# Kernel tuning notes

Measured on AMD Instinct MI355X. Metric: run time of the kernel, lower is better.

## Reference

```python
import jax, jax.numpy as jnp
import numpy as np

N_NODES = 20000
N_EDGES = 640000
IN_F = 128
CL1_F = 128
CL2_F = 128
OUT_F = 2


def setup_inputs() -> dict:
    key = jax.random.key(0)
    ks = jax.random.split(key, 8)
    x = jax.random.normal(ks[0], (N_NODES, IN_F), dtype=jnp.float32)
    edge_index = jax.random.randint(ks[1], (2, N_EDGES), 0, N_NODES, dtype=jnp.int64)
    s1 = 1.0 / np.sqrt(IN_F)
    s2 = 1.0 / np.sqrt(CL1_F)
    s3 = 1.0 / np.sqrt(CL2_F)
    W1 = jax.random.uniform(ks[2], (IN_F, CL1_F), jnp.float32, -s1, s1)
    b1 = jax.random.uniform(ks[3], (CL1_F,), jnp.float32, -s1, s1)
    W2 = jax.random.uniform(ks[4], (CL1_F, CL2_F), jnp.float32, -s2, s2)
    b2 = jax.random.uniform(ks[5], (CL2_F,), jnp.float32, -s2, s2)
    W3 = jax.random.uniform(ks[6], (CL2_F, OUT_F), jnp.float32, -s3, s3)
    b3 = jax.random.uniform(ks[7], (OUT_F,), jnp.float32, -s3, s3)
    return {"x": x, "edge_index": edge_index, "W1": W1, "b1": b1,
            "W2": W2, "b2": b2, "W3": W3, "b3": b3}


def _scatter_mean(feat_src, src, dst, n_nodes):
    # out[i] = mean over edges e with dst[e]==i of feat_src gathered at src[e]
    msg = feat_src[src]                                   # [E, F] gather
    summed = jax.ops.segment_sum(msg, dst, num_segments=n_nodes)  # [N, F]
    ones = jnp.ones((src.shape[0],), dtype=feat_src.dtype)
    cnt = jax.ops.segment_sum(ones, dst, num_segments=n_nodes)    # [N]
    return summed / jnp.maximum(cnt, 1.0)[:, None]


def _mpnn_layer(x, src, dst, W, b, n_nodes):
    aggr = _scatter_mean(x, src, dst, n_nodes)
    return jax.nn.relu(aggr @ W + b)


def reference(x, edge_index, W1, b1, W2, b2, W3, b3):
    src, dst = edge_index[0], edge_index[1]
    n = x.shape[0]
    h = _mpnn_layer(x, src, dst, W1, b1, n)   # conv1 (update relu); extra relu is no-op
    h = _mpnn_layer(h, src, dst, W2, b2, n)   # conv2
    # dropout in eval mode is identity
    return h @ W3 + b3
```

## Files before the change

kernel.cpp:

```cpp
#include <hip/hip_runtime.h>

#define N_NODES 20000
#define N_EDGES 640000
#define F 128
#define CAP 128
#define GEMM_BLOCKS (N_NODES / 32)
#define SCAT_BLOCKS 2560
#define SCAT_STRIDE (SCAT_BLOCKS / 8 * 256)
#define NODES_PER_XCD (N_NODES / 8)


__global__ __launch_bounds__(256)
void gemm_bucket_kernel(const float* __restrict__ A, const float* __restrict__ W,
                        float* __restrict__ C,
                        const int* __restrict__ src, const int* __restrict__ dst,
                        int* __restrict__ cnt, unsigned short* __restrict__ bucket) {
    __shared__ float As[32][F + 4];
    int tid = threadIdx.x;
    int bid = blockIdx.x;

    if (bid >= GEMM_BLOCKS) {
        int s   = bid - GEMM_BLOCKS;
        int g   = bid & 7;
        int idx = s >> 3;
        int lo  = g * NODES_PER_XCD;
        int hi  = lo + NODES_PER_XCD;
        for (int e = idx * 256 + tid; e < N_EDGES; e += SCAT_STRIDE) {
            int d  = dst[e];
            int sv = src[e];
            if (d >= lo && d < hi) {
                int pos = atomicAdd(&cnt[d], 1);
                if (pos < CAP) bucket[(size_t)d * CAP + pos] = (unsigned short)sv;
            }
        }
        return;
    }

    int row0 = bid * 32;
    const float4* A4 = (const float4*)(A + (size_t)row0 * F);
    for (int i = tid; i < 32 * 32; i += 256) {
        float4 v = A4[i];
        int r = i >> 5, c4 = (i & 31) * 4;
        *(float4*)&As[r][c4] = v;
    }
    __syncthreads();

    int tx = tid & 31, ty = tid >> 5;
    int c0 = tx * 4, r0 = ty * 4;
    float acc[4][4] = {};

    for (int k = 0; k < F; k += 4) {
        float4 a4[4];
#pragma unroll
        for (int i = 0; i < 4; ++i) a4[i] = *(const float4*)&As[r0 + i][k];
#pragma unroll
        for (int u = 0; u < 4; ++u) {
            float4 w = *(const float4*)(W + (size_t)(k + u) * F + c0);
#pragma unroll
            for (int i = 0; i < 4; ++i) {
                float a = (u == 0) ? a4[i].x : (u == 1) ? a4[i].y : (u == 2) ? a4[i].z : a4[i].w;
                acc[i][0] += a * w.x;
                acc[i][1] += a * w.y;
                acc[i][2] += a * w.z;
                acc[i][3] += a * w.w;
            }
        }
    }

#pragma unroll
    for (int i = 0; i < 4; ++i) {
        float4 o;
        o.x = acc[i][0]; o.y = acc[i][1]; o.z = acc[i][2]; o.w = acc[i][3];
        *(float4*)(C + (size_t)(row0 + r0 + i) * F + c0) = o;
    }
}

__global__ __launch_bounds__(256)
void gemm_kernel(const float* __restrict__ A, const float* __restrict__ W,
                 float* __restrict__ C) {
    __shared__ float As[32][F + 4];
    int tid  = threadIdx.x;
    int row0 = blockIdx.x * 32;

    const float4* A4 = (const float4*)(A + (size_t)row0 * F);
    for (int i = tid; i < 32 * 32; i += 256) {
        float4 v = A4[i];
        int r = i >> 5, c4 = (i & 31) * 4;
        *(float4*)&As[r][c4] = v;
    }
    __syncthreads();

    int tx = tid & 31, ty = tid >> 5;
    int c0 = tx * 4, r0 = ty * 4;
    float acc[4][4] = {};

    for (int k = 0; k < F; k += 4) {
        float4 a4[4];
#pragma unroll
        for (int i = 0; i < 4; ++i) a4[i] = *(const float4*)&As[r0 + i][k];
#pragma unroll
        for (int u = 0; u < 4; ++u) {
            float4 w = *(const float4*)(W + (size_t)(k + u) * F + c0);
#pragma unroll
            for (int i = 0; i < 4; ++i) {
                float a = (u == 0) ? a4[i].x : (u == 1) ? a4[i].y : (u == 2) ? a4[i].z : a4[i].w;
                acc[i][0] += a * w.x;
                acc[i][1] += a * w.y;
                acc[i][2] += a * w.z;
                acc[i][3] += a * w.w;
            }
        }
    }

#pragma unroll
    for (int i = 0; i < 4; ++i) {
        float4 o;
        o.x = acc[i][0]; o.y = acc[i][1]; o.z = acc[i][2]; o.w = acc[i][3];
        *(float4*)(C + (size_t)(row0 + r0 + i) * F + c0) = o;
    }
}

__device__ __forceinline__ float4 slice_gather(const float4* __restrict__ fb,
                                               int packed, int deg, int r) {
    float4 acc; acc.x = acc.y = acc.z = acc.w = 0.f;
    int nchunks = deg >> 3;
    int sh  = r >> 1;
    int sel = r & 1;
    int c = 0;
    for (; c + 4 <= nchunks; c += 4) {
        int w0 = __shfl(packed, (c << 2) + sh);
        int w1 = __shfl(packed, ((c + 1) << 2) + sh);
        int w2 = __shfl(packed, ((c + 2) << 2) + sh);
        int w3 = __shfl(packed, ((c + 3) << 2) + sh);
        int i0 = sel ? ((w0 >> 16) & 0xffff) : (w0 & 0xffff);
        int i1 = sel ? ((w1 >> 16) & 0xffff) : (w1 & 0xffff);
        int i2 = sel ? ((w2 >> 16) & 0xffff) : (w2 & 0xffff);
        int i3 = sel ? ((w3 >> 16) & 0xffff) : (w3 & 0xffff);
        float4 v0 = fb[(size_t)i0 * 32];
        float4 v1 = fb[(size_t)i1 * 32];
        float4 v2 = fb[(size_t)i2 * 32];
        float4 v3 = fb[(size_t)i3 * 32];
        acc.x += (v0.x + v1.x) + (v2.x + v3.x);
        acc.y += (v0.y + v1.y) + (v2.y + v3.y);
        acc.z += (v0.z + v1.z) + (v2.z + v3.z);
        acc.w += (v0.w + v1.w) + (v2.w + v3.w);
    }
    for (; c < nchunks; ++c) {
        int w = __shfl(packed, (c << 2) + sh);
        int idx = sel ? ((w >> 16) & 0xffff) : (w & 0xffff);
        float4 v = fb[(size_t)idx * 32];
        acc.x += v.x; acc.y += v.y; acc.z += v.z; acc.w += v.w;
    }
    int wt = __shfl(packed, (nchunks << 2) + sh);
    if (r < (deg & 7)) {
        int idx = sel ? ((wt >> 16) & 0xffff) : (wt & 0xffff);
        float4 v = fb[(size_t)idx * 32];
        acc.x += v.x; acc.y += v.y; acc.z += v.z; acc.w += v.w;
    }
    return acc;
}

__global__ __launch_bounds__(256)
void slice_agg_kernel(const float* __restrict__ y, const int* __restrict__ cnt,
                      const unsigned short* __restrict__ bucket,
                      const float* __restrict__ b, float* __restrict__ out) {
    int bid   = blockIdx.x;
    int g     = bid & 7;
    int i     = bid >> 3;
    int slice = g & 3;
    int jj    = i * 2 + (g >> 2);
    int wave  = threadIdx.x >> 6;
    int lane  = threadIdx.x & 63;
    int node0 = jj * 8 + wave * 2;
    int node1 = node0 + 1;
    int r     = lane >> 3;
    int c4    = lane & 7;

    int deg0 = cnt[node0];
    int deg1 = cnt[node1];
    const unsigned short* lst0 = bucket + (size_t)node0 * CAP;
    const unsigned short* lst1 = bucket + (size_t)node1 * CAP;
    int packed0 = *(const int*)(lst0 + 2 * lane);
    int packed1 = *(const int*)(lst1 + 2 * lane);

    const float4* fb = (const float4*)y + slice * 8 + c4;

    int d0 = deg0 < CAP ? deg0 : CAP;
    int d1 = deg1 < CAP ? deg1 : CAP;
    float4 a0 = slice_gather(fb, packed0, d0, r);
    float4 a1 = slice_gather(fb, packed1, d1, r);

#pragma unroll
    for (int off = 8; off < 64; off <<= 1) {
        a0.x += __shfl_xor(a0.x, off);
        a0.y += __shfl_xor(a0.y, off);
        a0.z += __shfl_xor(a0.z, off);
        a0.w += __shfl_xor(a0.w, off);
        a1.x += __shfl_xor(a1.x, off);
        a1.y += __shfl_xor(a1.y, off);
        a1.z += __shfl_xor(a1.z, off);
        a1.w += __shfl_xor(a1.w, off);
    }

    if (r == 0) {
        float4 bv = ((const float4*)b)[slice * 8 + c4];
        float inv0 = 1.0f / fmaxf((float)deg0, 1.0f);
        float4 o0;
        o0.x = fmaxf(a0.x * inv0 + bv.x, 0.f);
        o0.y = fmaxf(a0.y * inv0 + bv.y, 0.f);
        o0.z = fmaxf(a0.z * inv0 + bv.z, 0.f);
        o0.w = fmaxf(a0.w * inv0 + bv.w, 0.f);
        ((float4*)out)[(size_t)node0 * 32 + slice * 8 + c4] = o0;
        float inv1 = 1.0f / fmaxf((float)deg1, 1.0f);
        float4 o1;
        o1.x = fmaxf(a1.x * inv1 + bv.x, 0.f);
        o1.y = fmaxf(a1.y * inv1 + bv.y, 0.f);
        o1.z = fmaxf(a1.z * inv1 + bv.z, 0.f);
        o1.w = fmaxf(a1.w * inv1 + bv.w, 0.f);
        ((float4*)out)[(size_t)node1 * 32 + slice * 8 + c4] = o1;
    }
}

__global__ __launch_bounds__(256)
void final_kernel(const float* __restrict__ h, const float* __restrict__ W3,
                  const float* __restrict__ b3, float* __restrict__ out) {
    int wid  = (blockIdx.x * blockDim.x + threadIdx.x) >> 6;
    int lane = threadIdx.x & 63;
    if (wid >= N_NODES) return;
    float2 v = ((const float2*)h)[(size_t)wid * 64 + lane];
    float4 w = ((const float4*)W3)[lane];
    float a0 = v.x * w.x + v.y * w.z;
    float a1 = v.x * w.y + v.y * w.w;
#pragma unroll
    for (int off = 32; off > 0; off >>= 1) {
        a0 += __shfl_down(a0, off);
        a1 += __shfl_down(a1, off);
    }
    if (lane == 0) {
        out[(size_t)wid * 2]     = a0 + b3[0];
        out[(size_t)wid * 2 + 1] = a1 + b3[1];
    }
}

extern "C" void kernel_launch(void* const* d_in, const int* in_sizes, int n_in,
                              void* d_out, int out_size, void* d_ws, size_t ws_size,
                              hipStream_t stream) {
    const float* x   = (const float*)d_in[0];
    const int*   ei  = (const int*)d_in[1];
    const int*   src = ei;
    const int*   dst = ei + N_EDGES;
    const float* W1 = (const float*)d_in[2];
    const float* b1 = (const float*)d_in[3];
    const float* W2 = (const float*)d_in[4];
    const float* b2 = (const float*)d_in[5];
    const float* W3 = (const float*)d_in[6];
    const float* b3 = (const float*)d_in[7];
    float* out = (float*)d_out;

    char* base = (char*)d_ws;
    size_t off = 0;
    auto take = [&](size_t bytes) -> char* {
        char* p = base + off;
        off += (bytes + 255) & ~(size_t)255;
        return p;
    };
    int*            cnt    = (int*)           take(N_NODES * sizeof(int));
    unsigned short* bucket = (unsigned short*)take((size_t)N_NODES * CAP * sizeof(unsigned short));
    float*          y      = (float*)         take((size_t)N_NODES * F * sizeof(float));
    float*          h      = (float*)         take((size_t)N_NODES * F * sizeof(float));

    hipMemsetAsync(cnt, 0, N_NODES * sizeof(int), stream);

    gemm_bucket_kernel<<<GEMM_BLOCKS + SCAT_BLOCKS, 256, 0, stream>>>(
        x, W1, y, src, dst, cnt, bucket);
    slice_agg_kernel<<<N_NODES / 2, 256, 0, stream>>>(y, cnt, bucket, b1, h);
    gemm_kernel<<<N_NODES / 32, 256, 0, stream>>>(h, W2, y);
    slice_agg_kernel<<<N_NODES / 2, 256, 0, stream>>>(y, cnt, bucket, b2, h);
    final_kernel<<<(N_NODES * 64) / 256, 256, 0, stream>>>(h, W3, b3, out);
}
```

Measured before the change: 185.8 us.

## Map one node per 8-lane group in aggregation, drop cross-lane reduction

```diff
diff --git a/kernel.cpp b/kernel.cpp
--- a/kernel.cpp
+++ b/kernel.cpp
@@ -8,6 +8,7 @@
 #define SCAT_BLOCKS 2560
 #define SCAT_STRIDE (SCAT_BLOCKS / 8 * 256)
 #define NODES_PER_XCD (N_NODES / 8)
+#define AGG_BLOCKS 2504
 
 
 __global__ __launch_bounds__(256)
@@ -120,46 +121,6 @@
     }
 }
 
-__device__ __forceinline__ float4 slice_gather(const float4* __restrict__ fb,
-                                               int packed, int deg, int r) {
-    float4 acc; acc.x = acc.y = acc.z = acc.w = 0.f;
-    int nchunks = deg >> 3;
-    int sh  = r >> 1;
-    int sel = r & 1;
-    int c = 0;
-    for (; c + 4 <= nchunks; c += 4) {
-        int w0 = __shfl(packed, (c << 2) + sh);
-        int w1 = __shfl(packed, ((c + 1) << 2) + sh);
-        int w2 = __shfl(packed, ((c + 2) << 2) + sh);
-        int w3 = __shfl(packed, ((c + 3) << 2) + sh);
-        int i0 = sel ? ((w0 >> 16) & 0xffff) : (w0 & 0xffff);
-        int i1 = sel ? ((w1 >> 16) & 0xffff) : (w1 & 0xffff);
-        int i2 = sel ? ((w2 >> 16) & 0xffff) : (w2 & 0xffff);
-        int i3 = sel ? ((w3 >> 16) & 0xffff) : (w3 & 0xffff);
-        float4 v0 = fb[(size_t)i0 * 32];
-        float4 v1 = fb[(size_t)i1 * 32];
-        float4 v2 = fb[(size_t)i2 * 32];
-        float4 v3 = fb[(size_t)i3 * 32];
-        acc.x += (v0.x + v1.x) + (v2.x + v3.x);
-        acc.y += (v0.y + v1.y) + (v2.y + v3.y);
-        acc.z += (v0.z + v1.z) + (v2.z + v3.z);
-        acc.w += (v0.w + v1.w) + (v2.w + v3.w);
-    }
-    for (; c < nchunks; ++c) {
-        int w = __shfl(packed, (c << 2) + sh);
-        int idx = sel ? ((w >> 16) & 0xffff) : (w & 0xffff);
-        float4 v = fb[(size_t)idx * 32];
-        acc.x += v.x; acc.y += v.y; acc.z += v.z; acc.w += v.w;
-    }
-    int wt = __shfl(packed, (nchunks << 2) + sh);
-    if (r < (deg & 7)) {
-        int idx = sel ? ((wt >> 16) & 0xffff) : (wt & 0xffff);
-        float4 v = fb[(size_t)idx * 32];
-        acc.x += v.x; acc.y += v.y; acc.z += v.z; acc.w += v.w;
-    }
-    return acc;
-}
-
 __global__ __launch_bounds__(256)
 void slice_agg_kernel(const float* __restrict__ y, const int* __restrict__ cnt,
                       const unsigned short* __restrict__ bucket,
@@ -171,54 +132,52 @@
     int jj    = i * 2 + (g >> 2);
     int wave  = threadIdx.x >> 6;
     int lane  = threadIdx.x & 63;
-    int node0 = jj * 8 + wave * 2;
-    int node1 = node0 + 1;
     int r     = lane >> 3;
     int c4    = lane & 7;
 
-    int deg0 = cnt[node0];
-    int deg1 = cnt[node1];
-    const unsigned short* lst0 = bucket + (size_t)node0 * CAP;
-    const unsigned short* lst1 = bucket + (size_t)node1 * CAP;
-    int packed0 = *(const int*)(lst0 + 2 * lane);
-    int packed1 = *(const int*)(lst1 + 2 * lane);
+    int node_base = jj * 32 + wave * 8;
+    if (node_base >= N_NODES) return;
+    int node = node_base + r;
+
+    int deg = cnt[node];
+    int d   = deg < CAP ? deg : CAP;
+    const int* lst = (const int*)(bucket + (size_t)node * CAP);
 
     const float4* fb = (const float4*)y + slice * 8 + c4;
 
-    int d0 = deg0 < CAP ? deg0 : CAP;
-    int d1 = deg1 < CAP ? deg1 : CAP;
-    float4 a0 = slice_gather(fb, packed0, d0, r);
-    float4 a1 = slice_gather(fb, packed1, d1, r);
-
-#pragma unroll
-    for (int off = 8; off < 64; off <<= 1) {
-        a0.x += __shfl_xor(a0.x, off);
-        a0.y += __shfl_xor(a0.y, off);
-        a0.z += __shfl_xor(a0.z, off);
-        a0.w += __shfl_xor(a0.w, off);
-        a1.x += __shfl_xor(a1.x, off);
-        a1.y += __shfl_xor(a1.y, off);
-        a1.z += __shfl_xor(a1.z, off);
-        a1.w += __shfl_xor(a1.w, off);
-    }
-
-    if (r == 0) {
-        float4 bv = ((const float4*)b)[slice * 8 + c4];
-        float inv0 = 1.0f / fmaxf((float)deg0, 1.0f);
-        float4 o0;
-        o0.x = fmaxf(a0.x * inv0 + bv.x, 0.f);
-        o0.y = fmaxf(a0.y * inv0 + bv.y, 0.f);
-        o0.z = fmaxf(a0.z * inv0 + bv.z, 0.f);
-        o0.w = fmaxf(a0.w * inv0 + bv.w, 0.f);
-        ((float4*)out)[(size_t)node0 * 32 + slice * 8 + c4] = o0;
-        float inv1 = 1.0f / fmaxf((float)deg1, 1.0f);
-        float4 o1;
-        o1.x = fmaxf(a1.x * inv1 + bv.x, 0.f);
-        o1.y = fmaxf(a1.y * inv1 + bv.y, 0.f);
-        o1.z = fmaxf(a1.z * inv1 + bv.z, 0.f);
-        o1.w = fmaxf(a1.w * inv1 + bv.w, 0.f);
-        ((float4*)out)[(size_t)node1 * 32 + slice * 8 + c4] = o1;
-    }
+    float4 acc; acc.x = acc.y = acc.z = acc.w = 0.f;
+    int c = 0;
+    for (; c + 4 <= d; c += 4) {
+        int w0 = lst[c >> 1];
+        int w1 = lst[(c >> 1) + 1];
+        int i0 = w0 & 0xffff;
+        int i1 = (w0 >> 16) & 0xffff;
+        int i2 = w1 & 0xffff;
+        int i3 = (w1 >> 16) & 0xffff;
+        float4 v0 = fb[(size_t)i0 * 32];
+        float4 v1 = fb[(size_t)i1 * 32];
+        float4 v2 = fb[(size_t)i2 * 32];
+        float4 v3 = fb[(size_t)i3 * 32];
+        acc.x += (v0.x + v1.x) + (v2.x + v3.x);
+        acc.y += (v0.y + v1.y) + (v2.y + v3.y);
+        acc.z += (v0.z + v1.z) + (v2.z + v3.z);
+        acc.w += (v0.w + v1.w) + (v2.w + v3.w);
+    }
+    for (; c < d; ++c) {
+        int w   = lst[c >> 1];
+        int idx = (c & 1) ? ((w >> 16) & 0xffff) : (w & 0xffff);
+        float4 v = fb[(size_t)idx * 32];
+        acc.x += v.x; acc.y += v.y; acc.z += v.z; acc.w += v.w;
+    }
+
+    float4 bv = ((const float4*)b)[slice * 8 + c4];
+    float inv = 1.0f / fmaxf((float)deg, 1.0f);
+    float4 o;
+    o.x = fmaxf(acc.x * inv + bv.x, 0.f);
+    o.y = fmaxf(acc.y * inv + bv.y, 0.f);
+    o.z = fmaxf(acc.z * inv + bv.z, 0.f);
+    o.w = fmaxf(acc.w * inv + bv.w, 0.f);
+    ((float4*)out)[(size_t)node * 32 + slice * 8 + c4] = o;
 }
 
 __global__ __launch_bounds__(256)
@@ -273,8 +232,8 @@
 
     gemm_bucket_kernel<<<GEMM_BLOCKS + SCAT_BLOCKS, 256, 0, stream>>>(
         x, W1, y, src, dst, cnt, bucket);
-    slice_agg_kernel<<<N_NODES / 2, 256, 0, stream>>>(y, cnt, bucket, b1, h);
+    slice_agg_kernel<<<AGG_BLOCKS, 256, 0, stream>>>(y, cnt, bucket, b1, h);
     gemm_kernel<<<N_NODES / 32, 256, 0, stream>>>(h, W2, y);
-    slice_agg_kernel<<<N_NODES / 2, 256, 0, stream>>>(y, cnt, bucket, b2, h);
+    slice_agg_kernel<<<AGG_BLOCKS, 256, 0, stream>>>(y, cnt, bucket, b2, h);
     final_kernel<<<(N_NODES * 64) / 256, 256, 0, stream>>>(h, W3, b3, out);
 }
```

Result: slower. 189.9 us (+2.2%).
